# Optimization experiments

Measured on AMD Instinct MI355X. Metric: run time of the kernel, lower is better.

The kernel has to match this reference:

```python
import jax, jax.numpy as jnp
import numpy as np

GAMMA = 2.6
SIG0, SIG1 = 0.17, 4.86
EXP_S, EXP_F = 2.0, 0.6

F1_NP = np.array([[0.0025, 0.0125, 0.02, 0.0125, 0.0025],
                  [0.0125, 0.0625, 0.1, 0.0625, 0.0125],
                  [0.02, 0.1, 0.16, 0.1, 0.02],
                  [0.0125, 0.0625, 0.1, 0.0625, 0.0125],
                  [0.0025, 0.0125, 0.02, 0.0125, 0.0025]], dtype=np.float32)[None, None]
FILT0_NP = np.array([[0.04, 0.04, 0.05, 0.04, 0.04],
                     [0.04, 0.03, 0.04, 0.03, 0.04],
                     [0.05, 0.04, 0.05, 0.04, 0.05],
                     [0.04, 0.03, 0.04, 0.03, 0.04],
                     [0.04, 0.04, 0.05, 0.04, 0.04]], dtype=np.float32)[None, None]
FILT1_NP = np.zeros((5, 5), dtype=np.float32)
FILT1_NP[2, 2] = 1.0
FILT1_NP = FILT1_NP[None, None]


def _pad_rep(x, p):
    return jnp.pad(x, ((0, 0), (0, 0), (p, p), (p, p)), mode='edge')


def _conv(x, f, pad=0):
    return jax.lax.conv_general_dilated(
        x, f, window_strides=(1, 1), padding=[(pad, pad), (pad, pad)],
        dimension_numbers=('NCHW', 'OIHW', 'NCHW'))


def _down(img, f):
    # replicate-pad by 2, valid 5x5 conv (output same HxW), stride-2 subsample
    o = _conv(_pad_rep(img, 2), f)
    return o[:, :, ::2, ::2]


def _up(img, odd, f):
    x = _pad_rep(img, 1)
    B, C, Hp, Wp = x.shape
    h, w = 2 * Hp, 2 * Wp
    o = jnp.zeros((B, C, h, w), x.dtype).at[:, :, ::2, ::2].set(4.0 * x)
    o = _conv(o, f, pad=2)
    return o[:, :, 2:h - 2 - odd[0], 2:w - 2 - odd[1]]


def _laplacian_pyramid(img, n_lev, f):
    pyr = []
    o = img
    for _ in range(n_lev - 1):
        g = _down(o, f)
        odd = [g.shape[2] * 2 - o.shape[2], g.shape[3] * 2 - o.shape[3]]
        pyr.append(o - _up(g, odd, f))
        o = g
    pyr.append(o)
    return pyr


def _nlp(img, n_lev, F1, filt0, filt1):
    img = img ** (1.0 / GAMMA)
    pyr = _laplacian_pyramid(img, n_lev, F1)
    npyr = []
    for i in range(n_lev - 1):
        den = _conv(_pad_rep(jnp.abs(pyr[i]), 2), filt0) + SIG0
        npyr.append(pyr[i] / den)
    den = _conv(_pad_rep(jnp.abs(pyr[-1]), 2), filt1) + SIG1
    npyr.append(pyr[-1] / den)
    return npyr


def setup_inputs() -> dict:
    key = jax.random.key(0)
    k1, k2 = jax.random.split(key)
    B, H, W = 16, 512, 512
    h_img = jax.random.uniform(k1, (B, 1, H, W), dtype=jnp.float32)
    l_img = jax.random.uniform(k2, (B, 1, H, W), dtype=jnp.float32)
    return {
        'h_img': h_img,
        'l_img': l_img,
        'F1': jnp.asarray(F1_NP),
        'filt0': jnp.asarray(FILT0_NP),
        'filt1': jnp.asarray(FILT1_NP),
        'n_lev': 7,
    }


def reference(h_img, l_img, F1, filt0, filt1, n_lev):
    h_pyr = _nlp(h_img, n_lev, F1, filt0, filt1)
    l_pyr = _nlp(l_img, n_lev, F1, filt0, filt1)
    dis = []
    for i in range(n_lev):
        diff = jnp.abs(h_pyr[i] - l_pyr[i]) ** EXP_S
        dis.append(jnp.mean(diff, axis=(-2, -1)) ** (EXP_F / EXP_S))  # [B, 1]
    dis = jnp.concatenate(dis, axis=-1)  # [B, n_lev]
    loss = jnp.mean(dis, axis=-1) ** (1.0 / EXP_F)
    return jnp.mean(loss)
```

## Files before the change

kernel.cpp:

```cpp
#include <hip/hip_runtime.h>

#define SIG0 0.17f
#define SIG1 4.86f

__device__ __constant__ float c_filt0[25] = {
  0.04f,0.04f,0.05f,0.04f,0.04f,
  0.04f,0.03f,0.04f,0.03f,0.04f,
  0.05f,0.04f,0.05f,0.04f,0.05f,
  0.04f,0.03f,0.04f,0.03f,0.04f,
  0.04f,0.04f,0.05f,0.04f,0.04f};
__device__ __constant__ float c_f1d[5] = {0.05f,0.25f,0.4f,0.25f,0.05f};

static __device__ __forceinline__ int iclamp(int v, int lo, int hi){
  return v < lo ? lo : (v > hi ? hi : v);
}


struct FS {
  float sg[2][20][76];
  float s1[2][12][44];
  float red[4];
};
struct DS {
  float st[20][136];
  float hs[20][64];
};
struct TS {
  float A3[2][64][66];
  float A4[2][32][34];
  float A5[2][16][18];
  float A6[2][8][10];
  float red[4];
};

__device__ __forceinline__ void down_body(const float* __restrict__ in0, float* __restrict__ out0,
                                          int PSI, int PSO, int Sout, int xo0, int yo0, char* smem){
  DS* S = (DS*)smem;
  int tid = threadIdx.x;
  for (int f=tid; f<20*34; f+=256){
    int r=f/34, c4=f-34*r;
    *(float4*)&S->st[r][4*c4] = *(const float4*)&in0[(size_t)(2*yo0+r)*PSI + 2*xo0 + 4*c4];
  }
  __syncthreads();
  for (int f=tid; f<20*64; f+=256){
    int r=f>>6, xo=f&63;
    const float* rp = &S->st[r][2*xo+2];
    S->hs[r][xo] = 0.05f*rp[0]+0.25f*rp[1]+0.4f*rp[2]+0.25f*rp[3]+0.05f*rp[4];
  }
  __syncthreads();
  for (int f=tid; f<8*64; f+=256){
    int yo=f>>6, xo=f&63;
    int Y=yo0+yo, X=xo0+xo;
    float v = 0.05f*S->hs[2*yo][xo]+0.25f*S->hs[2*yo+1][xo]+0.4f*S->hs[2*yo+2][xo]
            +0.25f*S->hs[2*yo+3][xo]+0.05f*S->hs[2*yo+4][xo];
    int rlo=(Y==0)?0:(Y+2), rhi=(Y==Sout-1)?(Sout+3):(Y+2);
    int clo=(X==0)?0:(X+4), chi=(X==Sout-1)?(Sout+7):(X+4);
    for (int rr=rlo; rr<=rhi; rr++)
      for (int cc=clo; cc<=chi; cc++)
        out0[(size_t)rr*PSO+cc] = v;
  }
}

__global__ __launch_bounds__(256)
void k_d1(const float* __restrict__ hin, const float* __restrict__ lin,
          float* __restrict__ g1){
  __shared__ DS S;
  int xo0 = blockIdx.x*64, yo0 = blockIdx.y*8, z = blockIdx.z;
  const float* in = (z<16)? hin + (size_t)z*262144 : lin + (size_t)(z-16)*262144;
  float* out0 = g1 + (size_t)z*68640;
  int tid = threadIdx.x;
  const float e = 0.3846153846153846f;
  for (int f=tid; f<20*34; f+=256){
    int r=f/34, c4=f-34*r;
    int yy = iclamp(2*yo0-2+r, 0, 511);
    int xb = 2*xo0-4+4*c4;
    const float* rp = in + (size_t)yy*512;
    float4 v;
    if (xb>=0 && xb<=508) v = *(const float4*)&rp[xb];
    else { v.x=rp[iclamp(xb,0,511)]; v.y=rp[iclamp(xb+1,0,511)];
           v.z=rp[iclamp(xb+2,0,511)]; v.w=rp[iclamp(xb+3,0,511)]; }
    v.x=__powf(v.x,e); v.y=__powf(v.y,e); v.z=__powf(v.z,e); v.w=__powf(v.w,e);
    *(float4*)&S.st[r][4*c4] = v;
  }
  __syncthreads();
  for (int f=tid; f<20*64; f+=256){
    int r=f>>6, xo=f&63;
    const float* rp = &S.st[r][2*xo+2];
    S.hs[r][xo] = 0.05f*rp[0]+0.25f*rp[1]+0.4f*rp[2]+0.25f*rp[3]+0.05f*rp[4];
  }
  __syncthreads();
  for (int f=tid; f<8*64; f+=256){
    int yo=f>>6, xo=f&63;
    int Y=yo0+yo, X=xo0+xo;
    float v = 0.05f*S.hs[2*yo][xo]+0.25f*S.hs[2*yo+1][xo]+0.4f*S.hs[2*yo+2][xo]
            +0.25f*S.hs[2*yo+3][xo]+0.05f*S.hs[2*yo+4][xo];
    int rlo=(Y==0)?0:(Y+2), rhi=(Y==255)?259:(Y+2);
    int clo=(X==0)?0:(X+4), chi=(X==255)?263:(X+4);
    for (int rr=rlo; rr<=rhi; rr++)
      for (int cc=clo; cc<=chi; cc++)
        out0[(size_t)rr*264+cc] = v;
  }
}

template<int GAMMA>
__device__ __forceinline__ void fused_body(FS* S,
    const float* __restrict__ a0, const float* __restrict__ a1, int PS0,
    const float* __restrict__ s10, const float* __restrict__ s11, int PS1,
    int Simg, int x0, int y0, float* __restrict__ out_slot){
  int t = threadIdx.x;
  const float e = 0.3846153846153846f;

  if (t < 240){
    int img = t >= 120; int t2 = img ? t-120 : t;
    int r = t2/6, q3 = t2 - 6*r;
    float w[12];
    if (GAMMA){
      int yy = iclamp(y0-2+r, 0, 511);
      int xb = x0-4+12*q3;
      const float* rp = (img ? a1 : a0) + (size_t)yy*512;
      if (xb >= 0 && xb <= 500){
        *(float4*)&w[0] = *(const float4*)&rp[xb];
        *(float4*)&w[4] = *(const float4*)&rp[xb+4];
        *(float4*)&w[8] = *(const float4*)&rp[xb+8];
      } else {
        #pragma unroll
        for (int j=0;j<12;j++) w[j] = rp[iclamp(xb+j,0,511)];
      }
      #pragma unroll
      for (int j=0;j<12;j++) w[j] = __powf(w[j], e);
    } else {
      const float* rp = (img ? a1 : a0) + (size_t)(y0+r)*PS0 + x0 + 12*q3;
      *(float4*)&w[0] = *(const float4*)&rp[0];
      *(float4*)&w[4] = *(const float4*)&rp[4];
      *(float4*)&w[8] = *(const float4*)&rp[8];
    }
    float* dp = &S->sg[img][r][12*q3];
    *(float4*)&dp[0] = *(float4*)&w[0];
    *(float4*)&dp[4] = *(float4*)&w[4];
    *(float4*)&dp[8] = *(float4*)&w[8];
  }
  if (t < 240){
    int img = t >= 120; int t2 = img ? t-120 : t;
    int ro = t2/10, co = t2 - 10*ro;
    const float* src = (img ? s11 : s10) + (size_t)(y0/2+ro)*PS1 + x0/2 + 4*co;
    *(float4*)&S->s1[img][ro][4*co] = *(const float4*)src;
  }
  __syncthreads();

  {
    int tt = t & 127;
    bool ew = t < 128;
    if (tt < 120){
      int img = tt >= 60; int t2 = img ? tt-60 : tt;
      int rh = t2/6, q3 = t2 - 6*rh;
      int r = ew ? 2*rh : 2*rh+1;
      int cb = 6*q3;
      float B[12], C[12], u[12];
      {
        const float* pB = &S->s1[img][rh+1][cb];
        const float* pC = &S->s1[img][rh+2][cb];
        *(float4*)&B[0]=*(const float4*)&pB[0]; *(float4*)&B[4]=*(const float4*)&pB[4]; *(float4*)&B[8]=*(const float4*)&pB[8];
        *(float4*)&C[0]=*(const float4*)&pC[0]; *(float4*)&C[4]=*(const float4*)&pC[4]; *(float4*)&C[8]=*(const float4*)&pC[8];
      }
      if (ew){
        float A[12];
        const float* pA = &S->s1[img][rh][cb];
        *(float4*)&A[0]=*(const float4*)&pA[0]; *(float4*)&A[4]=*(const float4*)&pA[4]; *(float4*)&A[8]=*(const float4*)&pA[8];
        #pragma unroll
        for (int m=0;m<6;m++){
          float hEA = 0.05f*A[m+1]+0.4f*A[m+2]+0.05f*A[m+3];
          float hEB = 0.05f*B[m+1]+0.4f*B[m+2]+0.05f*B[m+3];
          float hEC = 0.05f*C[m+1]+0.4f*C[m+2]+0.05f*C[m+3];
          u[2*m]   = 0.2f*hEA + 1.6f*hEB + 0.2f*hEC;
          float hOA = 0.25f*(A[m+2]+A[m+3]);
          float hOB = 0.25f*(B[m+2]+B[m+3]);
          float hOC = 0.25f*(C[m+2]+C[m+3]);
          u[2*m+1] = 0.2f*hOA + 1.6f*hOB + 0.2f*hOC;
        }
      } else {
        #pragma unroll
        for (int m=0;m<6;m++){
          float hEB = 0.05f*B[m+1]+0.4f*B[m+2]+0.05f*B[m+3];
          float hEC = 0.05f*C[m+1]+0.4f*C[m+2]+0.05f*C[m+3];
          u[2*m]   = hEB + hEC;
          u[2*m+1] = 0.25f*(B[m+2]+B[m+3]) + 0.25f*(C[m+2]+C[m+3]);
        }
      }
      float* dp = &S->sg[img][r][12*q3];
      float v[12];
      *(float4*)&v[0]=*(float4*)&dp[0]; *(float4*)&v[4]=*(float4*)&dp[4]; *(float4*)&v[8]=*(float4*)&dp[8];
      #pragma unroll
      for (int j=0;j<12;j++) v[j] -= u[j];
      *(float4*)&dp[0]=*(float4*)&v[0]; *(float4*)&dp[4]=*(float4*)&v[4]; *(float4*)&dp[8]=*(float4*)&v[8];
    }
  }
  __syncthreads();

  bool top=(y0==0), bot=(y0+16==Simg), lft=(x0==0), rgt=(x0+64==Simg);
  if (top|bot|lft|rgt){
    for (int f=t; f<2*18; f+=256){
      int img = f>=18; int q = img ? f-18 : f;
      if (top){ float4 v=*(float4*)&S->sg[img][2][4*q];
                *(float4*)&S->sg[img][0][4*q]=v; *(float4*)&S->sg[img][1][4*q]=v; }
      if (bot){ float4 v=*(float4*)&S->sg[img][17][4*q];
                *(float4*)&S->sg[img][18][4*q]=v; *(float4*)&S->sg[img][19][4*q]=v; }
    }
    __syncthreads();
    for (int f=t; f<2*20; f+=256){
      int img = f>=20; int r = img ? f-20 : f;
      if (lft){ float v=S->sg[img][r][4];  float4 vv={v,v,v,v}; *(float4*)&S->sg[img][r][0]=vv; }
      if (rgt){ float v=S->sg[img][r][67]; float4 vv={v,v,v,v}; *(float4*)&S->sg[img][r][68]=vv; }
    }
    __syncthreads();
  }

  float vacc = 0.f;
  {
    int img = t & 1, quad = t >> 1;
    int qx = quad & 15, qy = quad >> 4;
    int cb = 4*qx, rb = 2*qy;
    float T0[4]={0,0,0,0}, T1[4]={0,0,0,0};
    float s5a[4], s5b[4], s3a[4], s3b[4], n0[4], n1[4];
    #pragma unroll
    for (int r=0;r<6;r++){
      float w[12];
      const float* rp = &S->sg[img][rb+r][cb];
      *(float4*)&w[0]=*(const float4*)&rp[0];
      *(float4*)&w[4]=*(const float4*)&rp[4];
      *(float4*)&w[8]=*(const float4*)&rp[8];
      float aw[8];
      #pragma unroll
      for (int j=0;j<8;j++) aw[j] = fabsf(w[j+2]);
      float h0 = ((aw[0]+aw[1])+(aw[2]+aw[3]))+aw[4];
      float h1 = h0 - aw[0] + aw[5];
      float h2 = h1 - aw[1] + aw[6];
      float h3 = h2 - aw[2] + aw[7];
      float hh[4] = {h0,h1,h2,h3};
      if (r<=4){
        #pragma unroll
        for (int c=0;c<4;c++) T0[c] += hh[c];
      }
      if (r>=1){
        #pragma unroll
        for (int c=0;c<4;c++) T1[c] += hh[c];
      }
      if (r==0){
        for (int c=0;c<4;c++) s5a[c] = aw[c+2];
      }
      if (r==1){
        for (int c=0;c<4;c++){ s3a[c] = aw[c+1]+aw[c+3]; s5b[c] = aw[c+2]; }
      }
      if (r==2){
        for (int c=0;c<4;c++){ s5a[c] += aw[c]+aw[c+2]+aw[c+4]; n0[c]=w[c+4]; s3b[c] = aw[c+1]+aw[c+3]; }
      }
      if (r==3){
        for (int c=0;c<4;c++){ s3a[c] += aw[c+1]+aw[c+3]; s5b[c] += aw[c]+aw[c+2]+aw[c+4]; n1[c]=w[c+4]; }
      }
      if (r==4){
        for (int c=0;c<4;c++){ s5a[c] += aw[c+2]; s3b[c] += aw[c+1]+aw[c+3]; }
      }
      if (r==5){
        for (int c=0;c<4;c++) s5b[c] += aw[c+2];
      }
    }
    float qv[8];
    #pragma unroll
    for (int c=0;c<4;c++){
      float d0 = SIG0 + 0.04f*T0[c] + 0.01f*s5a[c] - 0.01f*s3a[c];
      float d1 = SIG0 + 0.04f*T1[c] + 0.01f*s5b[c] - 0.01f*s3b[c];
      qv[c]   = __fdividef(n0[c], d0);
      qv[4+c] = __fdividef(n1[c], d1);
    }
    #pragma unroll
    for (int i=0;i<8;i++){
      float o = __shfl_xor(qv[i], 1);
      float d = qv[i] - o;
      vacc += d*d;
    }
    if (img) vacc = 0.f;
  }
  #pragma unroll
  for (int off=32; off>0; off>>=1) vacc += __shfl_down(vacc, off);
  if ((t&63)==0) S->red[t>>6] = vacc;
  __syncthreads();
  if (t==0)
    out_slot[0] = S->red[0]+S->red[1]+S->red[2]+S->red[3];
}

static __device__ __forceinline__ void down_lds(const float* Ain, int ldi, int Sin,
                                                float* Aout, int ldo, int Sout,
                                                int tid, int NT){
  int tot = 2*Sout*Sout;
  for (int f=tid; f<tot; f+=NT){
    int img = f/(Sout*Sout), rem = f%(Sout*Sout), y=rem/Sout, x=rem%Sout;
    const float* A = Ain + img*Sin*ldi;
    float s=0.f;
    #pragma unroll
    for (int i=0;i<5;i++){
      int yy=iclamp(2*y+i-2,0,Sin-1);
      float rs=0.f;
      #pragma unroll
      for (int j=0;j<5;j++){
        int xx=iclamp(2*x+j-2,0,Sin-1);
        rs += c_f1d[j]*A[yy*ldi+xx];
      }
      s += c_f1d[i]*rs;
    }
    Aout[img*Sout*ldo + y*ldo + x] = s;
  }
}

static __device__ __forceinline__ void lap_lds(float* Ak, int ldk, int S,
                                               const float* Ag, int ldg,
                                               int tid, int NT){
  int Sg = S>>1;
  int tot = 2*S*S;
  for (int f=tid; f<tot; f+=NT){
    int img=f/(S*S), rem=f%(S*S), y=rem/S, x=rem%S;
    const float* G = Ag + img*Sg*ldg;
    int y2=y>>1, x2=x>>1;
    int ry0,ry1,ry2; float wy0,wy1,wy2;
    if (!(y&1)){ ry0=iclamp(y2-1,0,Sg-1); ry1=y2; ry2=iclamp(y2+1,0,Sg-1); wy0=0.2f; wy1=1.6f; wy2=0.2f; }
    else { ry0=y2; ry1=iclamp(y2+1,0,Sg-1); ry2=y2; wy0=1.f; wy1=1.f; wy2=0.f; }
    int cx0,cx1,cx2; float wx0,wx1,wx2;
    if (!(x&1)){ cx0=iclamp(x2-1,0,Sg-1); cx1=x2; cx2=iclamp(x2+1,0,Sg-1); wx0=0.05f; wx1=0.4f; wx2=0.05f; }
    else { cx0=x2; cx1=iclamp(x2+1,0,Sg-1); cx2=x2; wx0=0.25f; wx1=0.25f; wx2=0.f; }
    float u0 = wx0*G[ry0*ldg+cx0]+wx1*G[ry0*ldg+cx1]+wx2*G[ry0*ldg+cx2];
    float u1 = wx0*G[ry1*ldg+cx0]+wx1*G[ry1*ldg+cx1]+wx2*G[ry1*ldg+cx2];
    float u2 = wx0*G[ry2*ldg+cx0]+wx1*G[ry2*ldg+cx1]+wx2*G[ry2*ldg+cx2];
    Ak[img*S*ldk + y*ldk + x] -= wy0*u0+wy1*u1+wy2*u2;
  }
}

static __device__ __forceinline__ float diff_lds(const float* A, int ld, int S,
                                                 int tid, int NT){
  float v=0.f;
  const float* Ah = A;
  const float* Al = A + S*ld;
  for (int f=tid; f<S*S; f+=NT){
    int y=f/S, x=f%S;
    float dh=SIG0, dl=SIG0;
    #pragma unroll
    for (int i=0;i<5;i++){
      int yy=iclamp(y+i-2,0,S-1);
      #pragma unroll
      for (int j=0;j<5;j++){
        int xx=iclamp(x+j-2,0,S-1);
        float w=c_filt0[i*5+j];
        dh += w*fabsf(Ah[yy*ld+xx]);
        dl += w*fabsf(Al[yy*ld+xx]);
      }
    }
    float d = __fdividef(Ah[y*ld+x],dh) - __fdividef(Al[y*ld+x],dl);
    v += d*d;
  }
  return v;
}

__device__ void tail_body(const float* __restrict__ g3, float* __restrict__ accum,
                          int b, char* smem){
  TS* T = (TS*)smem;
  int tid = threadIdx.x;
  const float* s0  = g3 + (size_t)b*4896 + 148;
  const float* s1p = g3 + (size_t)(b+16)*4896 + 148;
  for (int f=tid; f<2*4096; f+=256){
    int img=f>>12, rem=f&4095, r=rem>>6, c=rem&63;
    T->A3[img][r][c] = (img? s1p : s0)[(size_t)r*72+c];
  }
  __syncthreads();
  down_lds(&T->A3[0][0][0],66,64,&T->A4[0][0][0],34,32,tid,256);
  __syncthreads();
  down_lds(&T->A4[0][0][0],34,32,&T->A5[0][0][0],18,16,tid,256);
  __syncthreads();
  down_lds(&T->A5[0][0][0],18,16,&T->A6[0][0][0],10,8,tid,256);
  __syncthreads();
  lap_lds(&T->A3[0][0][0],66,64,&T->A4[0][0][0],34,tid,256);
  __syncthreads();
  float v3 = diff_lds(&T->A3[0][0][0],66,64,tid,256);
  lap_lds(&T->A4[0][0][0],34,32,&T->A5[0][0][0],18,tid,256);
  __syncthreads();
  float v4 = diff_lds(&T->A4[0][0][0],34,32,tid,256);
  lap_lds(&T->A5[0][0][0],18,16,&T->A6[0][0][0],10,tid,256);
  __syncthreads();
  float v5 = diff_lds(&T->A5[0][0][0],18,16,tid,256);
  float v6 = 0.f;
  for (int f=tid; f<64; f+=256){
    float ch = T->A6[0][f>>3][f&7];
    float cl = T->A6[1][f>>3][f&7];
    float d = __fdividef(ch, fabsf(ch)+SIG1) - __fdividef(cl, fabsf(cl)+SIG1);
    v6 += d*d;
  }
  float vs[4] = {v3, v4, v5, v6};
  #pragma unroll
  for (int k=0;k<4;k++){
    float v = vs[k];
    #pragma unroll
    for (int off=32; off>0; off>>=1) v += __shfl_down(v, off);
    if ((tid&63)==0) T->red[tid>>6] = v;
    __syncthreads();
    if (tid==0)
      accum[(3+k)*16 + b] = T->red[0]+T->red[1]+T->red[2]+T->red[3];
    __syncthreads();
  }
}

__global__ __launch_bounds__(256)
void k_d2(const float* __restrict__ h, const float* __restrict__ l,
          const float* __restrict__ g1, float* __restrict__ g2,
          float* __restrict__ p0){
  extern __shared__ char smem[];
  if (blockIdx.z < 16){
    int b = blockIdx.z, x0 = blockIdx.x*64, y0 = blockIdx.y*16;
    fused_body<1>((FS*)smem, h+(size_t)b*262144, l+(size_t)b*262144, 0,
                  g1+(size_t)b*68640, g1+(size_t)(b+16)*68640, 264,
                  512, x0, y0, p0 + b*256 + blockIdx.y*8 + blockIdx.x);
  } else {
    int id = (blockIdx.z-16)*256 + blockIdx.y*8 + blockIdx.x;
    int img = id>>5, rem = id&31, xt = rem&1, yt = rem>>1;
    down_body(g1+(size_t)img*68640, g2+(size_t)img*17952, 264, 136, 128, xt*64, yt*8, smem);
  }
}

__global__ __launch_bounds__(256)
void k_d4(const float* __restrict__ g1, float* __restrict__ g2,
          float* __restrict__ g3, float* __restrict__ p1){
  extern __shared__ char smem[];
  if (blockIdx.z < 16){
    int b = blockIdx.z, x0 = blockIdx.x*64, y0 = blockIdx.y*16;
    fused_body<0>((FS*)smem, g1+(size_t)b*68640, g1+(size_t)(b+16)*68640, 264,
                  g2+(size_t)b*17952, g2+(size_t)(b+16)*17952, 136,
                  256, x0, y0, p1 + b*64 + blockIdx.y*4 + blockIdx.x);
  } else {
    int id = (blockIdx.z-16)*64 + blockIdx.y*4 + blockIdx.x;
    int img = id>>3, yt = id&7;
    down_body(g2+(size_t)img*17952, g3+(size_t)img*4896, 136, 72, 64, 0, yt*8, smem);
  }
}

__global__ __launch_bounds__(256)
void k_d5(const float* __restrict__ g2, const float* __restrict__ g3,
          float* __restrict__ p2, float* __restrict__ accum){
  extern __shared__ char smem[];
  if (blockIdx.z < 16){
    int b = blockIdx.z, x0 = blockIdx.x*64, y0 = blockIdx.y*16;
    fused_body<0>((FS*)smem, g2+(size_t)b*17952, g2+(size_t)(b+16)*17952, 136,
                  g3+(size_t)b*4896, g3+(size_t)(b+16)*4896, 72,
                  128, x0, y0, p2 + b*16 + blockIdx.y*2 + blockIdx.x);
  } else {
    int id = blockIdx.y*2 + blockIdx.x;
    tail_body(g3, accum, id, smem);
  }
}

__global__ __launch_bounds__(256)
void k_d6(const float* __restrict__ p0, const float* __restrict__ p1,
          const float* __restrict__ p2, const float* __restrict__ accum,
          float* __restrict__ out){
  __shared__ float r0[16][16];
  __shared__ float r1[16][4];
  __shared__ float r2[16];
  __shared__ float fin[16];
  int t = threadIdx.x;
  {
    int b = t>>4, c = t&15;
    float s = 0.f;
    #pragma unroll
    for (int j=0;j<16;j++) s += p0[b*256 + c*16 + j];
    r0[b][c] = s;
  }
  if (t < 64){
    int b = t>>2, c = t&3;
    float s = 0.f;
    #pragma unroll
    for (int j=0;j<16;j++) s += p1[b*64 + c*16 + j];
    r1[b][c] = s;
  }
  if (t < 16){
    float s = 0.f;
    #pragma unroll
    for (int j=0;j<16;j++) s += p2[t*16 + j];
    r2[t] = s;
  }
  __syncthreads();
  if (t < 16){
    int b = t;
    float a0 = 0.f;
    #pragma unroll
    for (int c=0;c<16;c++) a0 += r0[b][c];
    float a1 = (r1[b][0]+r1[b][1])+(r1[b][2]+r1[b][3]);
    float a2 = r2[b];
    float m = powf(a0*(1.0f/262144.0f), 0.3f)
            + powf(a1*(1.0f/65536.0f), 0.3f)
            + powf(a2*(1.0f/16384.0f), 0.3f);
    #pragma unroll
    for (int k=3;k<7;k++){
      int hw = (512>>k)*(512>>k);
      m += powf(accum[k*16+b]/(float)hw, 0.3f);
    }
    m *= (1.0f/7.0f);
    fin[b] = powf(m, 1.6666666666666667f);
  }
  __syncthreads();
  if (t == 0){
    float s = 0.f;
    #pragma unroll
    for (int i=0;i<16;i++) s += fin[i];
    out[0] = s * (1.0f/16.0f);
  }
}

extern "C" void kernel_launch(void* const* d_in, const int* in_sizes, int n_in,
                              void* d_out, int out_size, void* d_ws, size_t ws_size,
                              hipStream_t stream){
  const float* h = (const float*)d_in[0];
  const float* l = (const float*)d_in[1];
  float* out = (float*)d_out;
  float* ws = (float*)d_ws;

  float* g1 = ws;
  float* g2 = g1 + 2196480;
  float* g3 = g2 + 574464;
  float* accum = g3 + 156672;
  float* p0 = accum + 112;
  float* p1 = p0 + 4096;
  float* p2 = p1 + 1024;

  size_t fsz = sizeof(FS) > sizeof(DS) ? sizeof(FS) : sizeof(DS);
  size_t tsz = sizeof(TS);

  k_d1<<<dim3(4,32,32), 256, 0, stream>>>(h, l, g1);
  k_d2<<<dim3(8,32,20), 256, fsz, stream>>>(h, l, g1, g2, p0);
  k_d4<<<dim3(4,16,20), 256, fsz, stream>>>(g1, g2, g3, p1);
  k_d5<<<dim3(2,8,17),  256, tsz, stream>>>(g2, g3, p2, accum);
  k_d6<<<1, 256, 0, stream>>>(p0, p1, p2, accum, out);
}
```

Measured before the change: 158.4 us.

## Split fused level-0 kernel from downsample and rework upsample thread mapping

Measured after the change: 163.0 us. 2.9% more time.

```diff
diff --git a/kernel.cpp b/kernel.cpp
--- a/kernel.cpp
+++ b/kernel.cpp
@@ -147,52 +147,44 @@
   }
   __syncthreads();
 
-  {
-    int tt = t & 127;
-    bool ew = t < 128;
-    if (tt < 120){
-      int img = tt >= 60; int t2 = img ? tt-60 : tt;
-      int rh = t2/6, q3 = t2 - 6*rh;
-      int r = ew ? 2*rh : 2*rh+1;
-      int cb = 6*q3;
-      float B[12], C[12], u[12];
-      {
-        const float* pB = &S->s1[img][rh+1][cb];
-        const float* pC = &S->s1[img][rh+2][cb];
-        *(float4*)&B[0]=*(const float4*)&pB[0]; *(float4*)&B[4]=*(const float4*)&pB[4]; *(float4*)&B[8]=*(const float4*)&pB[8];
-        *(float4*)&C[0]=*(const float4*)&pC[0]; *(float4*)&C[4]=*(const float4*)&pC[4]; *(float4*)&C[8]=*(const float4*)&pC[8];
-      }
-      if (ew){
-        float A[12];
-        const float* pA = &S->s1[img][rh][cb];
-        *(float4*)&A[0]=*(const float4*)&pA[0]; *(float4*)&A[4]=*(const float4*)&pA[4]; *(float4*)&A[8]=*(const float4*)&pA[8];
-        #pragma unroll
-        for (int m=0;m<6;m++){
-          float hEA = 0.05f*A[m+1]+0.4f*A[m+2]+0.05f*A[m+3];
-          float hEB = 0.05f*B[m+1]+0.4f*B[m+2]+0.05f*B[m+3];
-          float hEC = 0.05f*C[m+1]+0.4f*C[m+2]+0.05f*C[m+3];
-          u[2*m]   = 0.2f*hEA + 1.6f*hEB + 0.2f*hEC;
-          float hOA = 0.25f*(A[m+2]+A[m+3]);
-          float hOB = 0.25f*(B[m+2]+B[m+3]);
-          float hOC = 0.25f*(C[m+2]+C[m+3]);
-          u[2*m+1] = 0.2f*hOA + 1.6f*hOB + 0.2f*hOC;
-        }
-      } else {
-        #pragma unroll
-        for (int m=0;m<6;m++){
-          float hEB = 0.05f*B[m+1]+0.4f*B[m+2]+0.05f*B[m+3];
-          float hEC = 0.05f*C[m+1]+0.4f*C[m+2]+0.05f*C[m+3];
-          u[2*m]   = hEB + hEC;
-          u[2*m+1] = 0.25f*(B[m+2]+B[m+3]) + 0.25f*(C[m+2]+C[m+3]);
-        }
-      }
-      float* dp = &S->sg[img][r][12*q3];
-      float v[12];
-      *(float4*)&v[0]=*(float4*)&dp[0]; *(float4*)&v[4]=*(float4*)&dp[4]; *(float4*)&v[8]=*(float4*)&dp[8];
-      #pragma unroll
-      for (int j=0;j<12;j++) v[j] -= u[j];
-      *(float4*)&dp[0]=*(float4*)&v[0]; *(float4*)&dp[4]=*(float4*)&v[4]; *(float4*)&dp[8]=*(float4*)&v[8];
-    }
+  if (t < 180){
+    int img = t >= 90; int t2 = img ? t-90 : t;
+    int rp_ = t2/9, q = t2 - 9*rp_;
+    int cb1 = 4*q;
+    int cbg = 8*q;
+    float A[8], B[8], C[8];
+    *(float4*)&A[0] = *(const float4*)&S->s1[img][rp_  ][cb1];
+    *(float4*)&A[4] = *(const float4*)&S->s1[img][rp_  ][cb1+4];
+    *(float4*)&B[0] = *(const float4*)&S->s1[img][rp_+1][cb1];
+    *(float4*)&B[4] = *(const float4*)&S->s1[img][rp_+1][cb1+4];
+    *(float4*)&C[0] = *(const float4*)&S->s1[img][rp_+2][cb1];
+    *(float4*)&C[4] = *(const float4*)&S->s1[img][rp_+2][cb1+4];
+    float ue[8], uo[8];
+    #pragma unroll
+    for (int j=0;j<4;j++){
+      float hEA = 0.05f*A[j+1]+0.4f*A[j+2]+0.05f*A[j+3];
+      float hEB = 0.05f*B[j+1]+0.4f*B[j+2]+0.05f*B[j+3];
+      float hEC = 0.05f*C[j+1]+0.4f*C[j+2]+0.05f*C[j+3];
+      float hOA = 0.25f*(A[j+2]+A[j+3]);
+      float hOB = 0.25f*(B[j+2]+B[j+3]);
+      float hOC = 0.25f*(C[j+2]+C[j+3]);
+      ue[2*j]   = 0.2f*hEA + 1.6f*hEB + 0.2f*hEC;
+      ue[2*j+1] = 0.2f*hOA + 1.6f*hOB + 0.2f*hOC;
+      uo[2*j]   = hEB + hEC;
+      uo[2*j+1] = hOB + hOC;
+    }
+    float* dpe = &S->sg[img][2*rp_][cbg];
+    float ve[8];
+    *(float4*)&ve[0]=*(float4*)&dpe[0]; *(float4*)&ve[4]=*(float4*)&dpe[4];
+    #pragma unroll
+    for (int j=0;j<8;j++) ve[j] -= ue[j];
+    *(float4*)&dpe[0]=*(float4*)&ve[0]; *(float4*)&dpe[4]=*(float4*)&ve[4];
+    float* dpo = &S->sg[img][2*rp_+1][cbg];
+    float vo[8];
+    *(float4*)&vo[0]=*(float4*)&dpo[0]; *(float4*)&vo[4]=*(float4*)&dpo[4];
+    #pragma unroll
+    for (int j=0;j<8;j++) vo[j] -= uo[j];
+    *(float4*)&dpo[0]=*(float4*)&vo[0]; *(float4*)&dpo[4]=*(float4*)&vo[4];
   }
   __syncthreads();
 
@@ -405,20 +397,20 @@
 }
 
 __global__ __launch_bounds__(256)
-void k_d2(const float* __restrict__ h, const float* __restrict__ l,
-          const float* __restrict__ g1, float* __restrict__ g2,
-          float* __restrict__ p0){
+void k_fused0(const float* __restrict__ h, const float* __restrict__ l,
+              const float* __restrict__ g1, float* __restrict__ p0){
   extern __shared__ char smem[];
-  if (blockIdx.z < 16){
-    int b = blockIdx.z, x0 = blockIdx.x*64, y0 = blockIdx.y*16;
-    fused_body<1>((FS*)smem, h+(size_t)b*262144, l+(size_t)b*262144, 0,
-                  g1+(size_t)b*68640, g1+(size_t)(b+16)*68640, 264,
-                  512, x0, y0, p0 + b*256 + blockIdx.y*8 + blockIdx.x);
-  } else {
-    int id = (blockIdx.z-16)*256 + blockIdx.y*8 + blockIdx.x;
-    int img = id>>5, rem = id&31, xt = rem&1, yt = rem>>1;
-    down_body(g1+(size_t)img*68640, g2+(size_t)img*17952, 264, 136, 128, xt*64, yt*8, smem);
-  }
+  int b = blockIdx.z, x0 = blockIdx.x*64, y0 = blockIdx.y*16;
+  fused_body<1>((FS*)smem, h+(size_t)b*262144, l+(size_t)b*262144, 0,
+                g1+(size_t)b*68640, g1+(size_t)(b+16)*68640, 264,
+                512, x0, y0, p0 + b*256 + blockIdx.y*8 + blockIdx.x);
+}
+
+__global__ __launch_bounds__(256)
+void k_down1(const float* __restrict__ g1, float* __restrict__ g2){
+  extern __shared__ char smem[];
+  down_body(g1+(size_t)blockIdx.z*68640, g2+(size_t)blockIdx.z*17952, 264, 136, 128,
+            blockIdx.x*64, blockIdx.y*8, smem);
 }
 
 __global__ __launch_bounds__(256)
@@ -529,7 +521,8 @@
   size_t tsz = sizeof(TS);
 
   k_d1<<<dim3(4,32,32), 256, 0, stream>>>(h, l, g1);
-  k_d2<<<dim3(8,32,20), 256, fsz, stream>>>(h, l, g1, g2, p0);
+  k_fused0<<<dim3(8,32,16), 256, sizeof(FS), stream>>>(h, l, g1, p0);
+  k_down1<<<dim3(2,16,32), 256, sizeof(DS), stream>>>(g1, g2);
   k_d4<<<dim3(4,16,20), 256, fsz, stream>>>(g1, g2, g3, p1);
   k_d5<<<dim3(2,8,17),  256, tsz, stream>>>(g2, g3, p2, accum);
   k_d6<<<1, 256, 0, stream>>>(p0, p1, p2, accum, out);
```
